# Optimization experiments

Measured on AMD Instinct MI355X. Metric: run time of the kernel, lower is better.

The kernel has to match this reference:

```python
import jax, jax.numpy as jnp
import numpy as np

EMBED_DIM = 1024
NUM_HEADS = 16
HEAD_DIM = EMBED_DIM // NUM_HEADS
MAX_LEN = 1000  # default in RelativePositionalEncoding
B, T = 4, 1024


def setup_inputs() -> dict:
    key = jax.random.key(0)
    ks = jax.random.split(key, 12)
    s = 0.02
    d = EMBED_DIM
    return {
        "query": jax.random.normal(ks[0], (B, T, d), jnp.float32),
        "key": jax.random.normal(ks[1], (B, T, d), jnp.float32),
        "value": jax.random.normal(ks[2], (B, T, d), jnp.float32),
        "Wq": jax.random.normal(ks[3], (d, d), jnp.float32) * s,
        "bq": jnp.zeros((d,), jnp.float32),
        "Wk": jax.random.normal(ks[4], (d, d), jnp.float32) * s,
        "bk": jnp.zeros((d,), jnp.float32),
        "Wv": jax.random.normal(ks[5], (d, d), jnp.float32) * s,
        "bv": jnp.zeros((d,), jnp.float32),
        "Wo": jax.random.normal(ks[6], (d, d), jnp.float32) * s,
        "bo": jnp.zeros((d,), jnp.float32),
        "rel_emb": jax.random.normal(ks[7], (2 * MAX_LEN - 1, HEAD_DIM), jnp.float32) * s,
    }


def reference(query, key, value, Wq, bq, Wk, bk, Wv, bv, Wo, bo, rel_emb):
    Bq, Tq, C = query.shape
    H, hd = NUM_HEADS, HEAD_DIM
    # projections -> [B, H, T, hd]
    q = (query @ Wq.T + bq).reshape(Bq, Tq, H, hd).transpose(0, 2, 1, 3)
    k = (key @ Wk.T + bk).reshape(Bq, Tq, H, hd).transpose(0, 2, 1, 3)
    v = (value @ Wv.T + bv).reshape(Bq, Tq, H, hd).transpose(0, 2, 1, 3)
    # content scores [B, H, T, T]
    attn_scores = jnp.einsum('bhtd,bhsd->bhts', q, k)
    # relative positional embedding gather: E[t, s] = rel_emb[clamp(s - t + max_len - 1)]
    pos = jnp.arange(Tq)
    idx = jnp.clip(pos[None, :] - pos[:, None] + MAX_LEN - 1, 0, 2 * MAX_LEN - 2)
    E = rel_emb[idx]  # [T, T, hd]
    # NOTE: original uses raw (unprojected) query reshaped into heads for rel-pos scores
    rpe_q = query.transpose(1, 0, 2).reshape(Tq, Bq * H, hd)  # [T, B*H, hd]
    rpe = jnp.einsum('tnd,tsd->nts', rpe_q, E).reshape(Bq, H, Tq, Tq)
    # faithful to original: divide by scale = hd**-0.5 (i.e. multiply by sqrt(hd))
    scale = hd ** (-0.5)
    attn = (attn_scores + rpe) / scale
    attn_weights = jax.nn.softmax(attn, axis=-1)
    out = jnp.einsum('bhts,bhsd->bhtd', attn_weights, v)
    out = out.transpose(0, 2, 1, 3).reshape(Bq, Tq, C)
    return out @ Wo.T + bo
```

## Files before the change

kernel.cpp:

```cpp
#include <hip/hip_runtime.h>
#include <math.h>

typedef _Float16 h16;
typedef __attribute__((ext_vector_type(4))) _Float16 half4;
typedef __attribute__((ext_vector_type(8))) _Float16 half8;
typedef __attribute__((ext_vector_type(4))) float f32x4;

#define AS1 __attribute__((address_space(1)))
#define AS3 __attribute__((address_space(3)))
#define MFMA16(a, b, c) __builtin_amdgcn_mfma_f32_16x16x32_f16((a), (b), (c), 0, 0, 0)

__device__ __forceinline__ float ex2(float x) {
  return __builtin_amdgcn_exp2f(x);
}

template <int CTRL>
__device__ __forceinline__ float dppf(float x) {
  return __int_as_float(__builtin_amdgcn_update_dpp(
      0, __float_as_int(x), CTRL, 0xF, 0xF, true));
}
__device__ __forceinline__ float rmax16(float x) {
  x = fmaxf(x, dppf<0xB1>(x));
  x = fmaxf(x, dppf<0x4E>(x));
  x = fmaxf(x, dppf<0x124>(x));
  x = fmaxf(x, dppf<0x128>(x));
  return x;
}
__device__ __forceinline__ float rsum16(float x) {
  x += dppf<0xB1>(x);
  x += dppf<0x4E>(x);
  x += dppf<0x124>(x);
  x += dppf<0x128>(x);
  return x;
}

__global__ __launch_bounds__(256) void convert(
    const float* __restrict__ q, const float* __restrict__ k,
    const float* __restrict__ v, const float* __restrict__ Wq,
    const float* __restrict__ Wk, const float* __restrict__ Wv,
    const float* __restrict__ Wo, const float* __restrict__ rel, h16* q16c,
    h16* k16c, h16* v16c, h16* Wq16, h16* Wk16, h16* Wv16, h16* Wo16,
    h16* relb) {
  const int i = blockIdx.x * 256 + threadIdx.x;
  if (i >= 4226304) return;
  const float* src;
  h16* dst;
  int off;
  if (i < 1048576) {
    src = q; dst = q16c; off = i;
  } else if (i < 2097152) {
    src = k; dst = k16c; off = i - 1048576;
  } else if (i < 3145728) {
    src = v; dst = v16c; off = i - 2097152;
  } else if (i < 3407872) {
    src = Wq; dst = Wq16; off = i - 3145728;
  } else if (i < 3670016) {
    src = Wk; dst = Wk16; off = i - 3407872;
  } else if (i < 3932160) {
    src = Wv; dst = Wv16; off = i - 3670016;
  } else if (i < 4194304) {
    src = Wo; dst = Wo16; off = i - 3932160;
  } else {
    off = i - 4194304;
    half4 hv = (half4){(h16)0.f, (h16)0.f, (h16)0.f, (h16)0.f};
    if (off < 31984) {
      float4 f = *(const float4*)(rel + (size_t)off * 4);
      hv = (half4){(h16)f.x, (h16)f.y, (h16)f.z, (h16)f.w};
    }
    *(half4*)(relb + (size_t)off * 4) = hv;
    return;
  }
  float4 f = *(const float4*)(src + (size_t)off * 4);
  *(half4*)(dst + (size_t)off * 4) =
      (half4){(h16)f.x, (h16)f.y, (h16)f.z, (h16)f.w};
}

template <int MODE>
__device__ __forceinline__ void gemm128_body(const h16* __restrict__ A,
                                             const h16* __restrict__ Bt,
                                             const float* __restrict__ bias,
                                             h16* __restrict__ outp) {
  __shared__ alignas(16) h16 As[128 * 32];
  __shared__ alignas(16) h16 Bs[128 * 32];
  const int tid = threadIdx.x;
  const int wave = tid >> 6;
  const int lane = tid & 63;
  const int wm = wave >> 1, wn = wave & 1;
  const int tm0 = blockIdx.x * 128, tn0 = blockIdx.y * 128;
  const int lrow = lane & 15;
  const int kq = lane >> 4;
  const int srow = lane >> 2;
  const int scol = (lane & 3) * 8;

  f32x4 acc[4][4];
#pragma unroll
  for (int i = 0; i < 4; ++i)
#pragma unroll
    for (int j = 0; j < 4; ++j) acc[i][j] = (f32x4){0.f, 0.f, 0.f, 0.f};

  for (int k0 = 0; k0 < 1024; k0 += 32) {
    __syncthreads();
#pragma unroll
    for (int rep = 0; rep < 2; ++rep) {
      const int cw = wave * 2 + rep;
      const int row = cw * 16 + srow;
      __builtin_amdgcn_global_load_lds(
          (const AS1 void*)(A + (size_t)(tm0 + row) * 1024 + k0 + scol),
          (AS3 void*)(As + cw * 512), 16, 0, 0);
      __builtin_amdgcn_global_load_lds(
          (const AS1 void*)(Bt + (size_t)(tn0 + row) * 1024 + k0 + scol),
          (AS3 void*)(Bs + cw * 512), 16, 0, 0);
    }
    __syncthreads();
    half8 af[4], bf[4];
#pragma unroll
    for (int i = 0; i < 4; ++i)
      af[i] = *(const half8*)(As + (wm * 64 + i * 16 + lrow) * 32 + kq * 8);
#pragma unroll
    for (int j = 0; j < 4; ++j)
      bf[j] = *(const half8*)(Bs + (wn * 64 + j * 16 + lrow) * 32 + kq * 8);
#pragma unroll
    for (int i = 0; i < 4; ++i)
#pragma unroll
      for (int j = 0; j < 4; ++j) acc[i][j] = MFMA16(af[i], bf[j], acc[i][j]);
  }

#pragma unroll
  for (int j = 0; j < 4; ++j) {
    const int n = tn0 + wn * 64 + j * 16 + lrow;
    const float bval = bias[n];
#pragma unroll
    for (int i = 0; i < 4; ++i) {
      const int rowb = wm * 64 + i * 16 + kq * 4;
#pragma unroll
      for (int r = 0; r < 4; ++r) {
        const int m = tm0 + rowb + r;
        const float val = acc[i][j][r] + bval;
        const int b = m >> 10, t = m & 1023, hh = n >> 6, d = n & 63;
        if (MODE == 0) {
          outp[((size_t)((b << 4) + hh) << 16) + (t << 6) + d] = (h16)val;
        } else {
          outp[(((size_t)((b << 4) + hh) * 64 + d) << 10) + t] = (h16)val;
        }
      }
    }
  }
}

__global__ __launch_bounds__(256) void qkv_gemm(
    const h16* q16c, const h16* k16c, const h16* v16c, const h16* Wq16,
    const h16* Wk16, const h16* Wv16, const float* bq, const float* bk,
    const float* bv, h16* q16, h16* k16, h16* vt16) {
  const int z = blockIdx.z;
  const h16* A = (z == 0) ? q16c : (z == 1) ? k16c : v16c;
  const h16* Bt = (z == 0) ? Wq16 : (z == 1) ? Wk16 : Wv16;
  const float* bias = (z == 0) ? bq : (z == 1) ? bk : bv;
  if (z == 2)
    gemm128_body<1>(A, Bt, bias, vt16);
  else
    gemm128_body<0>(A, Bt, bias, (z == 0) ? q16 : k16);
}

__global__ __launch_bounds__(256) void out_gemm(const h16* __restrict__ A,
                                                const h16* __restrict__ Bt,
                                                const float* __restrict__ bo,
                                                float* __restrict__ out) {
  __shared__ alignas(16) h16 As[64 * 32];
  __shared__ alignas(16) h16 Bs[128 * 32];
  const int tid = threadIdx.x;
  const int wave = tid >> 6;
  const int lane = tid & 63;
  const int wm = wave >> 1, wn = wave & 1;
  const int tm0 = blockIdx.x * 64, tn0 = blockIdx.y * 128;
  const int lrow = lane & 15;
  const int kq = lane >> 4;
  const int srow = lane >> 2;
  const int scol = (lane & 3) * 8;

  f32x4 acc[2][4];
#pragma unroll
  for (int i = 0; i < 2; ++i)
#pragma unroll
    for (int j = 0; j < 4; ++j) acc[i][j] = (f32x4){0.f, 0.f, 0.f, 0.f};

  for (int k0 = 0; k0 < 1024; k0 += 32) {
    __syncthreads();
    {
      const int row = wave * 16 + srow;
      __builtin_amdgcn_global_load_lds(
          (const AS1 void*)(A + (size_t)(tm0 + row) * 1024 + k0 + scol),
          (AS3 void*)(As + wave * 512), 16, 0, 0);
    }
#pragma unroll
    for (int rep = 0; rep < 2; ++rep) {
      const int cw = wave * 2 + rep;
      const int row = cw * 16 + srow;
      __builtin_amdgcn_global_load_lds(
          (const AS1 void*)(Bt + (size_t)(tn0 + row) * 1024 + k0 + scol),
          (AS3 void*)(Bs + cw * 512), 16, 0, 0);
    }
    __syncthreads();
    half8 af[2], bf[4];
#pragma unroll
    for (int i = 0; i < 2; ++i)
      af[i] = *(const half8*)(As + (wm * 32 + i * 16 + lrow) * 32 + kq * 8);
#pragma unroll
    for (int j = 0; j < 4; ++j)
      bf[j] = *(const half8*)(Bs + (wn * 64 + j * 16 + lrow) * 32 + kq * 8);
#pragma unroll
    for (int i = 0; i < 2; ++i)
#pragma unroll
      for (int j = 0; j < 4; ++j) acc[i][j] = MFMA16(af[i], bf[j], acc[i][j]);
  }

#pragma unroll
  for (int j = 0; j < 4; ++j) {
    const int n = tn0 + wn * 64 + j * 16 + lrow;
    const float bval = bo[n];
#pragma unroll
    for (int i = 0; i < 2; ++i) {
      const int rowb = wm * 32 + i * 16 + kq * 4;
#pragma unroll
      for (int r = 0; r < 4; ++r) {
        const int m = tm0 + rowb + r;
        out[(size_t)m * 1024 + n] = acc[i][j][r] + bval;
      }
    }
  }
}

__global__ __launch_bounds__(256, 4) void attn_mfma(
    const h16* __restrict__ q16, const h16* __restrict__ k16,
    const h16* __restrict__ vt16, const h16* __restrict__ q16c,
    const h16* __restrict__ relb, h16* __restrict__ ao) {
  __shared__ alignas(16) h16 Kh[4096];
  __shared__ alignas(16) h16 Rl[8192];
  __shared__ alignas(16) h16 VtS[4096];
  __shared__ alignas(16) h16 Ps[4096];

  const int bid = blockIdx.x;
  const int ttile = bid & 15;
  const int bh = bid >> 4;
  const int b = bh >> 4, h = bh & 15;
  const int t0 = ttile << 6;
  const int tid = threadIdx.x;
  const int w = tid >> 6;
  const int lane = tid & 63;
  const int l15 = lane & 15;
  const int kq = lane >> 4;

  const int tq = t0 + w * 16 + l15;
  half8 aq[2], arq[2];
#pragma unroll
  for (int ks = 0; ks < 2; ++ks) {
    aq[ks] =
        *(const half8*)(q16 + ((size_t)bh * 1024 + tq) * 64 + kq * 8 + ks * 32);
    arq[ks] = *(const half8*)(q16c + ((size_t)(b * 1024 + tq)) * 1024 + h * 64 +
                              kq * 8 + ks * 32);
  }

  float m2[4], ls[4];
  f32x4 O[4];
#pragma unroll
  for (int r = 0; r < 4; ++r) {
    m2[r] = -1e30f;
    ls[r] = 0.f;
  }
#pragma unroll
  for (int db = 0; db < 4; ++db) O[db] = (f32x4){0.f, 0.f, 0.f, 0.f};

  const int trow = w * 16 + kq * 4;

  for (int s0 = 0; s0 < 1024; s0 += 64) {
    __syncthreads();

#pragma unroll
    for (int p = 0; p < 2; ++p) {
      const int a = (w * 2 + p) * 64 + lane;
      const int row = a >> 3;
      const int c = (a & 7) ^ (row & 7);
      __builtin_amdgcn_global_load_lds(
          (const AS1 void*)(k16 + ((size_t)(bh * 1024 + s0 + row)) * 64 +
                            c * 8),
          (AS3 void*)(Kh + (w * 2 + p) * 512), 16, 0, 0);
    }
#pragma unroll
    for (int p = 0; p < 2; ++p) {
      const int a = (w * 2 + p) * 64 + lane;
      const int row = a >> 3;
      const int c = (a & 7) ^ (row & 7);
      __builtin_amdgcn_global_load_lds(
          (const AS1 void*)(vt16 + ((size_t)(bh * 64 + row)) * 1024 + s0 +
                            c * 8),
          (AS3 void*)(VtS + (w * 2 + p) * 512), 16, 0, 0);
    }
    const int base = s0 - t0 + 999 - 63;
#pragma unroll
    for (int p = 0; p < 4; ++p) {
      const int a = (w * 4 + p) * 64 + lane;
      const int row = a >> 3;
      const int c = (a & 7) ^ (row & 7);
      int ridx = base + row;
      ridx = ridx < 0 ? 0 : (ridx > 1998 ? 1998 : ridx);
      __builtin_amdgcn_global_load_lds(
          (const AS1 void*)(relb + (size_t)ridx * 64 + c * 8),
          (AS3 void*)(Rl + (w * 4 + p) * 512), 16, 0, 0);
    }
    __syncthreads();

    __builtin_amdgcn_s_setprio(1);
    f32x4 S[4];
#pragma unroll
    for (int ns = 0; ns < 4; ++ns) {
      f32x4 s = (f32x4){0.f, 0.f, 0.f, 0.f};
      const int kr = ns * 16 + l15;
#pragma unroll
      for (int ks = 0; ks < 2; ++ks) {
        const int c = ((ks * 4 + kq) ^ (kr & 7)) << 3;
        s = MFMA16(aq[ks], *(const half8*)(Kh + kr * 64 + c), s);
      }
      S[ns] = s;
    }

    f32x4 G[5];
#pragma unroll
    for (int gi = 0; gi < 5; ++gi) {
      f32x4 g = (f32x4){0.f, 0.f, 0.f, 0.f};
      const int ur = (3 - w + gi) * 16 + l15;
#pragma unroll
      for (int ks = 0; ks < 2; ++ks) {
        const int c = ((ks * 4 + kq) ^ (ur & 7)) << 3;
        g = MFMA16(arq[ks], *(const half8*)(Rl + ur * 64 + c), g);
      }
      G[gi] = g;
    }
    __builtin_amdgcn_s_setprio(0);

    const float SC = 11.54156032711170727f;
#pragma unroll
    for (int r = 0; r < 4; ++r) {
      const int Cm = 15 - kq * 4 - r;
      const int sladdr = ((kq << 4) | ((l15 + Cm) & 15)) << 2;
      const bool nolap = (l15 >= Cm);
#pragma unroll
      for (int ns = 0; ns < 4; ++ns) {
        const float mv = nolap ? G[ns][r] : G[ns + 1][r];
        const float g = __int_as_float(
            __builtin_amdgcn_ds_bpermute(sladdr, __float_as_int(mv)));
        S[ns][r] = (S[ns][r] + g) * SC;
      }
    }

#pragma unroll
    for (int r = 0; r < 4; ++r) {
      float mx = fmaxf(fmaxf(S[0][r], S[1][r]), fmaxf(S[2][r], S[3][r]));
      mx = rmax16(mx);
      const float nm = fmaxf(m2[r], mx);
      const float al = ex2(m2[r] - nm);
      m2[r] = nm;
      const int t = trow + r;
      float rs = 0.f;
#pragma unroll
      for (int ns = 0; ns < 4; ++ns) {
        const float p = ex2(S[ns][r] - nm);
        rs += p;
        const int sl = ns * 16 + l15;
        Ps[t * 64 + (((sl >> 3) ^ (t & 7)) << 3) + (sl & 7)] = (h16)p;
      }
      rs = rsum16(rs);
      ls[r] = ls[r] * al + rs;
      O[0][r] *= al;
      O[1][r] *= al;
      O[2][r] *= al;
      O[3][r] *= al;
    }

    const int tp = w * 16 + l15;
    __builtin_amdgcn_s_setprio(1);
#pragma unroll
    for (int ks = 0; ks < 2; ++ks) {
      const int ca = ((ks * 4 + kq) ^ (tp & 7)) << 3;
      half8 pa = *(const half8*)(Ps + tp * 64 + ca);
#pragma unroll
      for (int db = 0; db < 4; ++db) {
        const int vr = db * 16 + l15;
        const int cb = ((ks * 4 + kq) ^ (vr & 7)) << 3;
        O[db] = MFMA16(pa, *(const half8*)(VtS + vr * 64 + cb), O[db]);
      }
    }
    __builtin_amdgcn_s_setprio(0);
  }

#pragma unroll
  for (int r = 0; r < 4; ++r) {
    const float inv = 1.f / ls[r];
    const int t = t0 + trow + r;
    h16* op = ao + ((size_t)(b * 1024 + t)) * 1024 + h * 64;
#pragma unroll
    for (int db = 0; db < 4; ++db) op[db * 16 + l15] = (h16)(O[db][r] * inv);
  }
}

extern "C" void kernel_launch(void* const* d_in, const int* in_sizes, int n_in,
                              void* d_out, int out_size, void* d_ws,
                              size_t ws_size, hipStream_t stream) {
  const float* query = (const float*)d_in[0];
  const float* key = (const float*)d_in[1];
  const float* value = (const float*)d_in[2];
  const float* Wq = (const float*)d_in[3];
  const float* bq = (const float*)d_in[4];
  const float* Wk = (const float*)d_in[5];
  const float* bk = (const float*)d_in[6];
  const float* Wv = (const float*)d_in[7];
  const float* bv = (const float*)d_in[8];
  const float* Wo = (const float*)d_in[9];
  const float* bo = (const float*)d_in[10];
  const float* rel = (const float*)d_in[11];

  char* ws = (char*)d_ws;
  h16* q16c = (h16*)ws;
  h16* k16c = (h16*)(ws + ((size_t)8 << 20));
  h16* v16c = (h16*)(ws + ((size_t)16 << 20));
  h16* Wq16 = (h16*)(ws + ((size_t)24 << 20));
  h16* Wk16 = (h16*)(ws + ((size_t)26 << 20));
  h16* Wv16 = (h16*)(ws + ((size_t)28 << 20));
  h16* Wo16 = (h16*)(ws + ((size_t)30 << 20));
  h16* q16 = (h16*)(ws + ((size_t)32 << 20));
  h16* k16 = (h16*)(ws + ((size_t)40 << 20));
  h16* vt16 = (h16*)(ws + ((size_t)48 << 20));
  h16* relb = (h16*)(ws + ((size_t)56 << 20));
  h16* ao = k16c;
  float* out = (float*)d_out;

  convert<<<16509, 256, 0, stream>>>(query, key, value, Wq, Wk, Wv, Wo, rel,
                                     q16c, k16c, v16c, Wq16, Wk16, Wv16, Wo16,
                                     relb);
  qkv_gemm<<<dim3(32, 8, 3), 256, 0, stream>>>(q16c, k16c, v16c, Wq16, Wk16,
                                               Wv16, bq, bk, bv, q16, k16,
                                               vt16);
  attn_mfma<<<1024, 256, 0, stream>>>(q16, k16, vt16, q16c, relb, ao);
  out_gemm<<<dim3(64, 8), 256, 0, stream>>>(ao, Wo16, bo, out);
}
```

Measured before the change: 257.6 us.

## Double-buffer K, V and relative-embedding tiles in attention kernel LDS

The attention kernel now keeps two LDS buffers each for the K, V^T and relative-embedding tiles. It issues the asynchronous global-to-LDS loads for the next key block before computing on the current one, which removes one barrier per iteration. The goal is to hide global load latency behind the MFMA and softmax work. In exchange, LDS use per block nearly doubles and the min-blocks launch bound is dropped, so fewer blocks may fit per CU. It also relies on the async loads having completed at the single remaining barrier.

```diff
diff --git a/kernel.cpp b/kernel.cpp
--- a/kernel.cpp
+++ b/kernel.cpp
@@ -229,13 +229,13 @@
   }
 }
 
-__global__ __launch_bounds__(256, 4) void attn_mfma(
+__global__ __launch_bounds__(256) void attn_mfma(
     const h16* __restrict__ q16, const h16* __restrict__ k16,
     const h16* __restrict__ vt16, const h16* __restrict__ q16c,
     const h16* __restrict__ relb, h16* __restrict__ ao) {
-  __shared__ alignas(16) h16 Kh[4096];
-  __shared__ alignas(16) h16 Rl[8192];
-  __shared__ alignas(16) h16 VtS[4096];
+  __shared__ alignas(16) h16 KhB[2][4096];
+  __shared__ alignas(16) h16 VtB[2][4096];
+  __shared__ alignas(16) h16 RlB[2][8192];
   __shared__ alignas(16) h16 Ps[4096];
 
   const int bid = blockIdx.x;
@@ -249,31 +249,7 @@
   const int l15 = lane & 15;
   const int kq = lane >> 4;
 
-  const int tq = t0 + w * 16 + l15;
-  half8 aq[2], arq[2];
-#pragma unroll
-  for (int ks = 0; ks < 2; ++ks) {
-    aq[ks] =
-        *(const half8*)(q16 + ((size_t)bh * 1024 + tq) * 64 + kq * 8 + ks * 32);
-    arq[ks] = *(const half8*)(q16c + ((size_t)(b * 1024 + tq)) * 1024 + h * 64 +
-                              kq * 8 + ks * 32);
-  }
-
-  float m2[4], ls[4];
-  f32x4 O[4];
-#pragma unroll
-  for (int r = 0; r < 4; ++r) {
-    m2[r] = -1e30f;
-    ls[r] = 0.f;
-  }
-#pragma unroll
-  for (int db = 0; db < 4; ++db) O[db] = (f32x4){0.f, 0.f, 0.f, 0.f};
-
-  const int trow = w * 16 + kq * 4;
-
-  for (int s0 = 0; s0 < 1024; s0 += 64) {
-    __syncthreads();
-
+  const auto stage = [&](int buf, int s0) {
 #pragma unroll
     for (int p = 0; p < 2; ++p) {
       const int a = (w * 2 + p) * 64 + lane;
@@ -282,7 +258,7 @@
       __builtin_amdgcn_global_load_lds(
           (const AS1 void*)(k16 + ((size_t)(bh * 1024 + s0 + row)) * 64 +
                             c * 8),
-          (AS3 void*)(Kh + (w * 2 + p) * 512), 16, 0, 0);
+          (AS3 void*)(&KhB[buf][(w * 2 + p) * 512]), 16, 0, 0);
     }
 #pragma unroll
     for (int p = 0; p < 2; ++p) {
@@ -292,9 +268,9 @@
       __builtin_amdgcn_global_load_lds(
           (const AS1 void*)(vt16 + ((size_t)(bh * 64 + row)) * 1024 + s0 +
                             c * 8),
-          (AS3 void*)(VtS + (w * 2 + p) * 512), 16, 0, 0);
-    }
-    const int base = s0 - t0 + 999 - 63;
+          (AS3 void*)(&VtB[buf][(w * 2 + p) * 512]), 16, 0, 0);
+    }
+    const int base = s0 - t0 + 936;
 #pragma unroll
     for (int p = 0; p < 4; ++p) {
       const int a = (w * 4 + p) * 64 + lane;
@@ -304,9 +280,42 @@
       ridx = ridx < 0 ? 0 : (ridx > 1998 ? 1998 : ridx);
       __builtin_amdgcn_global_load_lds(
           (const AS1 void*)(relb + (size_t)ridx * 64 + c * 8),
-          (AS3 void*)(Rl + (w * 4 + p) * 512), 16, 0, 0);
-    }
+          (AS3 void*)(&RlB[buf][(w * 4 + p) * 512]), 16, 0, 0);
+    }
+  };
+
+  const int tq = t0 + w * 16 + l15;
+  half8 aq[2], arq[2];
+#pragma unroll
+  for (int ks = 0; ks < 2; ++ks) {
+    aq[ks] =
+        *(const half8*)(q16 + ((size_t)bh * 1024 + tq) * 64 + kq * 8 + ks * 32);
+    arq[ks] = *(const half8*)(q16c + ((size_t)(b * 1024 + tq)) * 1024 + h * 64 +
+                              kq * 8 + ks * 32);
+  }
+
+  float m2[4], ls[4];
+  f32x4 O[4];
+#pragma unroll
+  for (int r = 0; r < 4; ++r) {
+    m2[r] = -1e30f;
+    ls[r] = 0.f;
+  }
+#pragma unroll
+  for (int db = 0; db < 4; ++db) O[db] = (f32x4){0.f, 0.f, 0.f, 0.f};
+
+  const int trow = w * 16 + kq * 4;
+
+  stage(0, 0);
+
+  for (int t = 0; t < 16; ++t) {
     __syncthreads();
+    const int cur = t & 1;
+    if (t < 15) stage(cur ^ 1, (t + 1) * 64);
+
+    const h16* Kh = KhB[cur];
+    const h16* VtS = VtB[cur];
+    const h16* Rl = RlB[cur];
 
     __builtin_amdgcn_s_setprio(1);
     f32x4 S[4];
@@ -358,14 +367,14 @@
       const float nm = fmaxf(m2[r], mx);
       const float al = ex2(m2[r] - nm);
       m2[r] = nm;
-      const int t = trow + r;
+      const int t2 = trow + r;
       float rs = 0.f;
 #pragma unroll
       for (int ns = 0; ns < 4; ++ns) {
         const float p = ex2(S[ns][r] - nm);
         rs += p;
         const int sl = ns * 16 + l15;
-        Ps[t * 64 + (((sl >> 3) ^ (t & 7)) << 3) + (sl & 7)] = (h16)p;
+        Ps[t2 * 64 + (((sl >> 3) ^ (t2 & 7)) << 3) + (sl & 7)] = (h16)p;
       }
       rs = rsum16(rs);
       ls[r] = ls[r] * al + rs;
```

New measurement: 263.5 us. +2.3%, slower.
